# Kernel optimization log

Measured on AMD Instinct MI355X. Metric: run time of the kernel, lower is better.

Reference implementation:

```python
import jax, jax.numpy as jnp
import numpy as np

B, L, DIM, K, V = 512, 200, 256, 2048, 100000


def setup_inputs() -> dict:
    key = jax.random.key(0)
    k1, k2, k3, k4, k5 = jax.random.split(key, 5)
    return {
        "history_item_ids": jax.random.randint(k1, (B, L), 0, V, dtype=jnp.int32),
        "history_item_masks": jax.random.randint(k2, (B, L), 0, 3, dtype=jnp.int32),
        "embedding_table": jax.random.normal(k3, (V, DIM), dtype=jnp.float32) * 0.1,
        "code_book": jax.random.normal(k4, (K, DIM), dtype=jnp.float32) * 0.1,
        "W_enc": jax.random.normal(k5, (2 * DIM, DIM), dtype=jnp.float32) * 0.05,
        "b_enc": jnp.zeros((DIM,), dtype=jnp.float32),
    }


def reference(history_item_ids, history_item_masks, embedding_table, code_book, W_enc, b_enc):
    # mask: valid history positions (>= 1)
    mask = (history_item_masks >= 1).astype(jnp.float32)            # [B, L]
    emb = embedding_table[history_item_ids] * mask[:, :, None]      # [B, L, D]
    # masked mean over history (eps matches the tf 1e-9)
    hist_mean = emb.sum(axis=1) / (mask.sum(axis=1, keepdims=True) + 1e-9)  # [B, D]
    # VQ quantization: pairwise squared distances, argmin, codebook gather
    flat = emb.reshape(-1, emb.shape[-1])                           # [B*L, D]
    distances = (
        jnp.sum(flat * flat, axis=1, keepdims=True)
        + jnp.sum(code_book * code_book, axis=1)
        - 2.0 * flat @ code_book.T
    )                                                               # [B*L, K]
    idx = jnp.argmin(distances, axis=1)                             # [B*L]
    vq = code_book[idx].reshape(emb.shape)                          # [B, L, D] (== one_hot @ code_book)
    vq_mean = vq.sum(axis=1) / mask.sum(axis=-1)[:, None]           # [B, D] (no eps in tf vqvae)
    x = jnp.concatenate([vq_mean, hist_mean], axis=-1)              # [B, 2D]
    return x @ W_enc + b_enc                                        # encoder dense -> [B, D]
```

## Files before the change

### kernel.cpp

```cpp
#include <hip/hip_runtime.h>
#include <hip/hip_bf16.h>
#include <cstddef>
#include <cstdint>

#define B_  512
#define L_  200
#define D_  256
#define K_  2048
#define BL_ (B_ * L_)

typedef __bf16 bf16x8 __attribute__((ext_vector_type(8)));
typedef float  f32x16 __attribute__((ext_vector_type(16)));

#define GL_LDS(g, l) __builtin_amdgcn_global_load_lds(                          \
    (const __attribute__((address_space(1))) void*)(g),                         \
    (__attribute__((address_space(3))) void*)(l), 16, 0, 0)

__device__ inline ushort f2bf(float f) {
    union { float f; uint u; } a; a.f = f;
    uint r = a.u + 0x7FFFu + ((a.u >> 16) & 1u);
    return (ushort)(r >> 16);
}

__global__ __launch_bounds__(256) void prep_kernel(const float* __restrict__ cb,
                                                   float* __restrict__ cnorm,
                                                   float* __restrict__ cnormR,
                                                   ushort* __restrict__ cbbf) {
    int code = (blockIdx.x * 256 + threadIdx.x) >> 6;
    int lane = threadIdx.x & 63;
    float4 v = ((const float4*)(cb + (size_t)code * D_))[lane];
    float s = v.x * v.x + v.y * v.y + v.z * v.z + v.w * v.w;
    #pragma unroll
    for (int off = 32; off; off >>= 1) s += __shfl_down(s, off);
    union { ushort us[4]; uint2 u2; } pk;
    pk.us[0] = f2bf(v.x); pk.us[1] = f2bf(v.y); pk.us[2] = f2bf(v.z); pk.us[3] = f2bf(v.w);
    ((uint2*)(cbbf + (size_t)code * D_))[lane] = pk.u2;
    if (lane == 0) {
        cnorm[code] = s;
        int r = code & 31;
        int h = (r >> 2) & 1;
        int j = (r & 3) | ((r >> 3) << 2);
        cnormR[(code & ~31) | (h << 4) | j] = s + 16.0f;
    }
}

__global__ __launch_bounds__(256) void kstar_kernel(const float* __restrict__ cnorm,
                                                    int* __restrict__ kstar) {
    __shared__ unsigned long long red[4];
    const int t = threadIdx.x;
    unsigned long long best = ~0ull;
    #pragma unroll
    for (int i = 0; i < K_ / 256; ++i) {
        int k = i * 256 + t;
        unsigned long long key = (((unsigned long long)__float_as_uint(cnorm[k])) << 11) | (unsigned)k;
        best = best < key ? best : key;
    }
    #pragma unroll
    for (int off = 32; off; off >>= 1) {
        unsigned long long o = __shfl_down(best, off);
        best = best < o ? best : o;
    }
    if ((t & 63) == 0) red[t >> 6] = best;
    __syncthreads();
    if (t == 0) {
        unsigned long long b = red[0];
        for (int i = 1; i < 4; ++i) b = b < red[i] ? b : red[i];
        kstar[0] = (int)(b & 0x7FFull);
    }
}

struct CN4 { float4 a, b, c, d; };

__device__ inline CN4 ldcn(const float* p) {
    CN4 r;
    r.a = ((const float4*)p)[0];
    r.b = ((const float4*)p)[1];
    r.c = ((const float4*)p)[2];
    r.d = ((const float4*)p)[3];
    return r;
}

#define STAGE(CIDX, BUF) {                                                      \
    int wub = __builtin_amdgcn_readfirstlane((t >> 6) * 256);                   \
    _Pragma("unroll")                                                           \
    for (int i_ = 0; i_ < 4; ++i_) {                                            \
      int slot = wub + i_ * 64 + (t & 63);                                      \
      int n_ = slot >> 5, up_ = slot & 31;                                      \
      int u_ = up_ ^ (n_ & 7);                                                  \
      GL_LDS(cbbf + (((size_t)(((CIDX) << 5) + n_)) << 8) + (u_ << 3),          \
             (char*)(BUF) + (size_t)(wub + i_ * 64) * 16);                      \
    } }

#define PROCSEL(BUF, NC, CN) {                                                  \
    f32x16 A0, A1;                                                              \
    A0[0]=(CN).a.x; A0[1]=(CN).a.y; A0[2]=(CN).a.z; A0[3]=(CN).a.w;             \
    A0[4]=(CN).b.x; A0[5]=(CN).b.y; A0[6]=(CN).b.z; A0[7]=(CN).b.w;             \
    A0[8]=(CN).c.x; A0[9]=(CN).c.y; A0[10]=(CN).c.z; A0[11]=(CN).c.w;           \
    A0[12]=(CN).d.x; A0[13]=(CN).d.y; A0[14]=(CN).d.z; A0[15]=(CN).d.w;         \
    A1 = A0;                                                                    \
    _Pragma("unroll")                                                           \
    for (int s_ = 0; s_ < 16; ++s_) {                                           \
      bf16x8 aF = *(const bf16x8*)((const char*)(BUF) +                         \
                    (((l31 << 5) + ((2 * s_ + h) ^ swz)) << 4));                \
      A0 = __builtin_amdgcn_mfma_f32_32x32x16_bf16(aF, bfrag[0][s_], A0, 0,0,0);\
      A1 = __builtin_amdgcn_mfma_f32_32x32x16_bf16(aF, bfrag[1][s_], A1, 0,0,0);\
    }                                                                           \
    uint sb_ = (uint)((NC) << 5);                                               \
    _Pragma("unroll")                                                           \
    for (int jp_ = 0; jp_ < 8; ++jp_) {                                         \
      int j0_ = 2 * jp_, j1_ = 2 * jp_ + 1;                                     \
      uint c0_ = sb_ + (uint)((j0_ & 3) + 8 * (j0_ >> 2));                      \
      uint c1_ = sb_ + (uint)((j1_ & 3) + 8 * (j1_ >> 2));                      \
      {                                                                         \
        uint ka = (__float_as_uint(A0[j0_]) & 0xFFFFF800u) | (c0_ + h4);        \
        uint kb = (__float_as_uint(A0[j1_]) & 0xFFFFF800u) | (c1_ + h4);        \
        uint lo = min(ka, kb), hi = max(ka, kb);                                \
        uint tt = max(b1a, lo);                                                 \
        b1a = min(b1a, lo);                                                     \
        b2a = min(min(b2a, tt), hi);                                            \
      }                                                                         \
      {                                                                         \
        uint ka = (__float_as_uint(A1[j0_]) & 0xFFFFF800u) | (c0_ + h4);        \
        uint kb = (__float_as_uint(A1[j1_]) & 0xFFFFF800u) | (c1_ + h4);        \
        uint lo = min(ka, kb), hi = max(ka, kb);                                \
        uint tt = max(b1b, lo);                                                 \
        b1b = min(b1b, lo);                                                     \
        b2b = min(min(b2b, tt), hi);                                            \
      }                                                                         \
    } }

__global__ __launch_bounds__(256, 2) void gemm_top2_kernel(
    const int* __restrict__ ids, const int* __restrict__ masks,
    const float* __restrict__ table, const ushort* __restrict__ cbbf,
    const float* __restrict__ cnormR, uint2* __restrict__ cand) {

  __shared__ ushort cbuf0[32 * 256];
  __shared__ ushort cbuf1[32 * 256];

  const int t    = threadIdx.x;
  const int lane = t & 63;
  const int l31  = lane & 31;
  const int h    = lane >> 5;
  const int w    = t >> 6;
  const int ptile = blockIdx.x;
  const int swz  = l31 & 7;
  const uint h4  = (uint)(h << 2);

  bf16x8 bfrag[2][16];
  #pragma unroll
  for (int pt = 0; pt < 2; ++pt) {
    int pos = ptile * 256 + w * 64 + pt * 32 + l31;
    int id  = ids[pos];
    float m = (masks[pos] >= 1) ? -2.0f : 0.0f;
    const float* er = table + (size_t)id * D_ + 8 * h;
    #pragma unroll
    for (int s = 0; s < 16; ++s) {
      float4 x = *(const float4*)(er + 16 * s);
      float4 y = *(const float4*)(er + 16 * s + 4);
      bf16x8 b;
      b[0] = (__bf16)(x.x * m); b[1] = (__bf16)(x.y * m);
      b[2] = (__bf16)(x.z * m); b[3] = (__bf16)(x.w * m);
      b[4] = (__bf16)(y.x * m); b[5] = (__bf16)(y.y * m);
      b[6] = (__bf16)(y.z * m); b[7] = (__bf16)(y.w * m);
      bfrag[pt][s] = b;
    }
  }

  uint b1a = 0xFFFFFFFFu, b2a = 0xFFFFFFFFu;
  uint b1b = 0xFFFFFFFFu, b2b = 0xFFFFFFFFu;

  const float* cnh = cnormR;
  CN4 cnA = ldcn(cnh + 0 * 32 + h * 16);
  STAGE(0, cbuf0);
  __syncthreads();

  #pragma unroll 1
  for (int nc = 0; nc < 64; nc += 2) {
    CN4 cnB = ldcn(cnh + (nc + 1) * 32 + h * 16);
    STAGE(nc + 1, cbuf1);
    PROCSEL(cbuf0, nc, cnA);
    __syncthreads();
    if (nc + 2 < 64) {
      cnA = ldcn(cnh + (nc + 2) * 32 + h * 16);
      STAGE(nc + 2, cbuf0);
    }
    PROCSEL(cbuf1, nc + 1, cnB);
    __syncthreads();
  }

  {
    uint ob1 = __shfl_xor(b1a, 32), ob2 = __shfl_xor(b2a, 32);
    uint m1 = min(b1a, ob1);
    uint m2 = min(min(max(b1a, ob1), b2a), ob2);
    if (h == 0) cand[(size_t)(ptile * 256 + w * 64 + 0 * 32 + l31)] = make_uint2(m1, m2);
  }
  {
    uint ob1 = __shfl_xor(b1b, 32), ob2 = __shfl_xor(b2b, 32);
    uint m1 = min(b1b, ob1);
    uint m2 = min(min(max(b1b, ob1), b2b), ob2);
    if (h == 0) cand[(size_t)(ptile * 256 + w * 64 + 1 * 32 + l31)] = make_uint2(m1, m2);
  }
}

#define GRP 5

__global__ __launch_bounds__(256, 1) void tail_kernel(
    const int* __restrict__ ids, const int* __restrict__ masks,
    const float* __restrict__ table, const float* __restrict__ cb,
    const float* __restrict__ cnorm, const uint2* __restrict__ cand2,
    const int* __restrict__ kstar,
    float* __restrict__ gacc, int* __restrict__ gcnt) {

    __shared__ float red_vq[4][D_];
    __shared__ float red_e[4][D_];
    __shared__ int   redc[4];

    const int b    = blockIdx.x >> 1;
    const int half = blockIdx.x & 1;
    const int t = threadIdx.x;
    const int wv = t >> 6, lane = t & 63;

    const int ks = kstar[0];
    float4 ckstar = ((const float4*)(cb + (size_t)ks * D_))[lane];

    float4 vqa = make_float4(0.f, 0.f, 0.f, 0.f);
    float4 ea  = make_float4(0.f, 0.f, 0.f, 0.f);
    int cnta = 0, mcnt = 0;

    #pragma unroll 1
    for (int g = 0; g < 25 / GRP; ++g) {
        const int l0 = half * 100 + wv * 25 + g * GRP;

        uint2 kk[GRP];
        int   id[GRP];
        int   mk[GRP];
        #pragma unroll
        for (int j = 0; j < GRP; ++j) {
            int u = b * L_ + l0 + j;
            kk[j] = cand2[u];
            id[j] = ids[u];
            mk[j] = masks[u];
        }

        int k1[GRP], k2[GRP];
        bool valid[GRP], needy[GRP];
        #pragma unroll
        for (int j = 0; j < GRP; ++j) {
            uint g1 = kk[j].x;
            uint g2 = kk[j].y;
            k1[j] = (int)(g1 & 0x7FFu);
            k2[j] = (int)(g2 & 0x7FFu);
            valid[j] = (mk[j] >= 1);
            needy[j] = valid[j] && (((g2 & 0xFFFFF800u) - (g1 & 0xFFFFF800u)) < (3u << 11));
        }

        float4 e[GRP], c1[GRP], c2[GRP];
        #pragma unroll
        for (int j = 0; j < GRP; ++j)
            if (valid[j]) e[j] = ((const float4*)(table + (size_t)id[j] * D_))[lane];
        #pragma unroll
        for (int j = 0; j < GRP; ++j)
            if (valid[j]) c1[j] = ((const float4*)(cb + (size_t)k1[j] * D_))[lane];
        #pragma unroll
        for (int j = 0; j < GRP; ++j)
            if (needy[j]) c2[j] = ((const float4*)(cb + (size_t)k2[j] * D_))[lane];

        #pragma unroll
        for (int j = 0; j < GRP; ++j) {
            if (!valid[j]) { mcnt++; continue; }
            float4 ch = c1[j];
            if (needy[j]) {
                float d1 = fmaf(e[j].x, c1[j].x, fmaf(e[j].y, c1[j].y,
                            fmaf(e[j].z, c1[j].z, e[j].w * c1[j].w)));
                float d2 = fmaf(e[j].x, c2[j].x, fmaf(e[j].y, c2[j].y,
                            fmaf(e[j].z, c2[j].z, e[j].w * c2[j].w)));
                #pragma unroll
                for (int off = 32; off; off >>= 1) {
                    d1 += __shfl_xor(d1, off);
                    d2 += __shfl_xor(d2, off);
                }
                float s1 = cnorm[k1[j]] - 2.0f * d1;
                float s2 = cnorm[k2[j]] - 2.0f * d2;
                bool sel = (s2 < s1) || (s2 == s1 && k2[j] < k1[j]);
                ch = sel ? c2[j] : c1[j];
            }
            vqa.x += ch.x; vqa.y += ch.y; vqa.z += ch.z; vqa.w += ch.w;
            ea.x += e[j].x; ea.y += e[j].y; ea.z += e[j].z; ea.w += e[j].w;
            cnta++;
        }
    }

    float fm = (float)mcnt;
    vqa.x = fmaf(fm, ckstar.x, vqa.x);
    vqa.y = fmaf(fm, ckstar.y, vqa.y);
    vqa.z = fmaf(fm, ckstar.z, vqa.z);
    vqa.w = fmaf(fm, ckstar.w, vqa.w);

    *(float4*)&red_vq[wv][lane * 4] = vqa;
    *(float4*)&red_e[wv][lane * 4]  = ea;
    if (lane == 0) redc[wv] = cnta;
    __syncthreads();

    float vs = red_vq[0][t] + red_vq[1][t] + red_vq[2][t] + red_vq[3][t];
    float es = red_e[0][t] + red_e[1][t] + red_e[2][t] + red_e[3][t];
    atomicAdd(&gacc[(size_t)b * (2 * D_) + t], vs);
    atomicAdd(&gacc[(size_t)b * (2 * D_) + D_ + t], es);
    if (t == 0) atomicAdd(&gcnt[b], redc[0] + redc[1] + redc[2] + redc[3]);
}

__global__ __launch_bounds__(256) void dense_kernel(
    const float* __restrict__ gacc, const int* __restrict__ gcnt,
    const float* __restrict__ W, const float* __restrict__ bvec,
    float* __restrict__ out) {

    __shared__ float x[2 * D_];
    const int b = blockIdx.x;
    const int t = threadIdx.x;

    float fc = (float)gcnt[b];
    x[t]      = gacc[(size_t)b * (2 * D_) + t] / fc;
    x[D_ + t] = gacc[(size_t)b * (2 * D_) + D_ + t] / (fc + 1e-9f);
    __syncthreads();

    float acc = bvec[t];
    #pragma unroll 8
    for (int i = 0; i < 2 * D_; ++i)
        acc = fmaf(x[i], W[i * D_ + t], acc);
    out[(size_t)b * D_ + t] = acc;
}

extern "C" void kernel_launch(void* const* d_in, const int* in_sizes, int n_in,
                              void* d_out, int out_size, void* d_ws, size_t ws_size,
                              hipStream_t stream) {
    const int*   ids   = (const int*)  d_in[0];
    const int*   masks = (const int*)  d_in[1];
    const float* table = (const float*)d_in[2];
    const float* cb    = (const float*)d_in[3];
    const float* W     = (const float*)d_in[4];
    const float* bvec  = (const float*)d_in[5];
    float* out = (float*)d_out;

    char* p = (char*)d_ws;
    float*  cnorm  = (float*)p;             p += 8192;
    float*  cnormR = (float*)p;             p += 8192;
    ushort* cbbf   = (ushort*)p;            p += 1048576;
    uint2*  cand   = (uint2*)p;             p += (size_t)BL_ * 16;
    float*  gacc   = (float*)p;             p += (size_t)B_ * 2 * D_ * 4;
    int*    gcnt   = (int*)p;               p += B_ * 4;
    int*    kstar  = (int*)p;               p += 64;

    hipMemsetAsync(gacc, 0, (size_t)B_ * 2 * D_ * 4 + B_ * 4, stream);

    prep_kernel<<<K_ * 64 / 256, 256, 0, stream>>>(cb, cnorm, cnormR, cbbf);
    kstar_kernel<<<1, 256, 0, stream>>>(cnorm, kstar);
    gemm_top2_kernel<<<BL_ / 256, 256, 0, stream>>>(ids, masks, table, cbbf, cnormR, cand);
    tail_kernel<<<B_ * 2, 256, 0, stream>>>(ids, masks, table, cb, cnorm,
                                            cand, kstar, gacc, gcnt);
    dense_kernel<<<B_, 256, 0, stream>>>(gacc, gcnt, W, bvec, out);
}
```

Before: 317.7 us.

## Quad-buffer codebook staging with vmcnt waits and preload code norms into LDS

Replaces the double-buffered codebook chunk staging, which used two __syncthreads per pair of chunks, with a 4-buffer ring that prefetches three chunks ahead. Each iteration now does a single s_waitcnt vmcnt plus s_barrier. Per-chunk code-norm vectors are loaded once into LDS via global_load_lds instead of from global memory each chunk. This aims to hide load latency and remove barrier stalls, at the cost of more LDS (72KB vs 32KB), which may limit occupancy to fewer blocks per CU.

```diff
diff --git a/kernel.cpp b/kernel.cpp
--- a/kernel.cpp
+++ b/kernel.cpp
@@ -71,16 +71,7 @@
 
 struct CN4 { float4 a, b, c, d; };
 
-__device__ inline CN4 ldcn(const float* p) {
-    CN4 r;
-    r.a = ((const float4*)p)[0];
-    r.b = ((const float4*)p)[1];
-    r.c = ((const float4*)p)[2];
-    r.d = ((const float4*)p)[3];
-    return r;
-}
-
-#define STAGE(CIDX, BUF) {                                                      \
+#define STAGE(CIDX, BASE) {                                                     \
     int wub = __builtin_amdgcn_readfirstlane((t >> 6) * 256);                   \
     _Pragma("unroll")                                                           \
     for (int i_ = 0; i_ < 4; ++i_) {                                            \
@@ -88,10 +79,10 @@
       int n_ = slot >> 5, up_ = slot & 31;                                      \
       int u_ = up_ ^ (n_ & 7);                                                  \
       GL_LDS(cbbf + (((size_t)(((CIDX) << 5) + n_)) << 8) + (u_ << 3),          \
-             (char*)(BUF) + (size_t)(wub + i_ * 64) * 16);                      \
+             (char*)(BASE) + (size_t)(wub + i_ * 64) * 16);                     \
     } }
 
-#define PROCSEL(BUF, NC, CN) {                                                  \
+#define PROCSEL(BASE, NC, CN) {                                                 \
     f32x16 A0, A1;                                                              \
     A0[0]=(CN).a.x; A0[1]=(CN).a.y; A0[2]=(CN).a.z; A0[3]=(CN).a.w;             \
     A0[4]=(CN).b.x; A0[5]=(CN).b.y; A0[6]=(CN).b.z; A0[7]=(CN).b.w;             \
@@ -100,7 +91,7 @@
     A1 = A0;                                                                    \
     _Pragma("unroll")                                                           \
     for (int s_ = 0; s_ < 16; ++s_) {                                           \
-      bf16x8 aF = *(const bf16x8*)((const char*)(BUF) +                         \
+      bf16x8 aF = *(const bf16x8*)((const char*)(BASE) +                        \
                     (((l31 << 5) + ((2 * s_ + h) ^ swz)) << 4));                \
       A0 = __builtin_amdgcn_mfma_f32_32x32x16_bf16(aF, bfrag[0][s_], A0, 0,0,0);\
       A1 = __builtin_amdgcn_mfma_f32_32x32x16_bf16(aF, bfrag[1][s_], A1, 0,0,0);\
@@ -129,13 +120,17 @@
       }                                                                         \
     } }
 
+#define LDCN_LDS(NC, CN) {                                                      \
+    const float4* cp_ = (const float4*)(cnlds + ((NC) << 5) + (h << 4));        \
+    (CN).a = cp_[0]; (CN).b = cp_[1]; (CN).c = cp_[2]; (CN).d = cp_[3]; }
+
 __global__ __launch_bounds__(256, 2) void gemm_top2_kernel(
     const int* __restrict__ ids, const int* __restrict__ masks,
     const float* __restrict__ table, const ushort* __restrict__ cbbf,
     const float* __restrict__ cnormR, uint2* __restrict__ cand) {
 
-  __shared__ ushort cbuf0[32 * 256];
-  __shared__ ushort cbuf1[32 * 256];
+  __shared__ ushort cbuf[4 * 32 * 256];
+  __shared__ float  cnlds[2048];
 
   const int t    = threadIdx.x;
   const int lane = t & 63;
@@ -169,23 +164,47 @@
   uint b1a = 0xFFFFFFFFu, b2a = 0xFFFFFFFFu;
   uint b1b = 0xFFFFFFFFu, b2b = 0xFFFFFFFFu;
 
-  const float* cnh = cnormR;
-  CN4 cnA = ldcn(cnh + 0 * 32 + h * 16);
-  STAGE(0, cbuf0);
-  __syncthreads();
+  asm volatile("s_waitcnt vmcnt(0)" ::: "memory");
+  __builtin_amdgcn_sched_barrier(0);
+
+  {
+    int wub2 = __builtin_amdgcn_readfirstlane((t >> 6) * 128);
+    #pragma unroll
+    for (int i = 0; i < 2; ++i) {
+      int slot = wub2 + i * 64 + (t & 63);
+      GL_LDS(cnormR + (size_t)slot * 4, (char*)cnlds + (size_t)(wub2 + i * 64) * 16);
+    }
+  }
+  STAGE(0, (char*)cbuf);
+  STAGE(1, (char*)cbuf + 16384);
+  STAGE(2, (char*)cbuf + 32768);
 
   #pragma unroll 1
-  for (int nc = 0; nc < 64; nc += 2) {
-    CN4 cnB = ldcn(cnh + (nc + 1) * 32 + h * 16);
-    STAGE(nc + 1, cbuf1);
-    PROCSEL(cbuf0, nc, cnA);
-    __syncthreads();
-    if (nc + 2 < 64) {
-      cnA = ldcn(cnh + (nc + 2) * 32 + h * 16);
-      STAGE(nc + 2, cbuf0);
-    }
-    PROCSEL(cbuf1, nc + 1, cnB);
-    __syncthreads();
+  for (int nc = 0; nc < 62; ++nc) {
+    asm volatile("s_waitcnt vmcnt(8)" ::: "memory");
+    __builtin_amdgcn_s_barrier();
+    __builtin_amdgcn_sched_barrier(0);
+    if (nc <= 60) {
+      char* sb = (char*)cbuf + (size_t)(((nc + 3) & 3) * 16384);
+      STAGE(nc + 3, sb);
+    }
+    CN4 cn; LDCN_LDS(nc, cn);
+    char* rb = (char*)cbuf + (size_t)((nc & 3) * 16384);
+    PROCSEL(rb, nc, cn);
+  }
+  {
+    asm volatile("s_waitcnt vmcnt(4)" ::: "memory");
+    __builtin_amdgcn_s_barrier();
+    __builtin_amdgcn_sched_barrier(0);
+    CN4 cn; LDCN_LDS(62, cn);
+    PROCSEL((char*)cbuf + (size_t)((62 & 3) * 16384), 62, cn);
+  }
+  {
+    asm volatile("s_waitcnt vmcnt(0)" ::: "memory");
+    __builtin_amdgcn_s_barrier();
+    __builtin_amdgcn_sched_barrier(0);
+    CN4 cn; LDCN_LDS(63, cn);
+    PROCSEL((char*)cbuf + (size_t)((63 & 3) * 16384), 63, cn);
   }
 
   {
```

Result: no change. 314.4 us (-1.0%).

## Process two codebook chunks per pipeline stage and prefetch before embedding load

Applied to the files above, without the earlier changes.

Each double-buffer stage now holds two 32-code chunks (64 codes) instead of one, so the main loop runs half as many iterations and barriers, with four independent MFMA accumulator chains per step. The first codebook stage is issued before the embedding gather so that load overlaps fragment construction. This doubles LDS use per block (64 KB total) and adds accumulator registers, which may cut occupancy below the two blocks per CU the launch bounds request.

```diff
diff --git a/kernel.cpp b/kernel.cpp
--- a/kernel.cpp
+++ b/kernel.cpp
@@ -80,7 +80,7 @@
     return r;
 }
 
-#define STAGE(CIDX, BUF) {                                                      \
+#define STAGE(CIDX, BASE) {                                                     \
     int wub = __builtin_amdgcn_readfirstlane((t >> 6) * 256);                   \
     _Pragma("unroll")                                                           \
     for (int i_ = 0; i_ < 4; ++i_) {                                            \
@@ -88,23 +88,20 @@
       int n_ = slot >> 5, up_ = slot & 31;                                      \
       int u_ = up_ ^ (n_ & 7);                                                  \
       GL_LDS(cbbf + (((size_t)(((CIDX) << 5) + n_)) << 8) + (u_ << 3),          \
-             (char*)(BUF) + (size_t)(wub + i_ * 64) * 16);                      \
+             (char*)(BASE) + (size_t)(wub + i_ * 64) * 16);                     \
     } }
 
-#define PROCSEL(BUF, NC, CN) {                                                  \
-    f32x16 A0, A1;                                                              \
-    A0[0]=(CN).a.x; A0[1]=(CN).a.y; A0[2]=(CN).a.z; A0[3]=(CN).a.w;             \
-    A0[4]=(CN).b.x; A0[5]=(CN).b.y; A0[6]=(CN).b.z; A0[7]=(CN).b.w;             \
-    A0[8]=(CN).c.x; A0[9]=(CN).c.y; A0[10]=(CN).c.z; A0[11]=(CN).c.w;           \
-    A0[12]=(CN).d.x; A0[13]=(CN).d.y; A0[14]=(CN).d.z; A0[15]=(CN).d.w;         \
-    A1 = A0;                                                                    \
-    _Pragma("unroll")                                                           \
-    for (int s_ = 0; s_ < 16; ++s_) {                                           \
-      bf16x8 aF = *(const bf16x8*)((const char*)(BUF) +                         \
-                    (((l31 << 5) + ((2 * s_ + h) ^ swz)) << 4));                \
-      A0 = __builtin_amdgcn_mfma_f32_32x32x16_bf16(aF, bfrag[0][s_], A0, 0,0,0);\
-      A1 = __builtin_amdgcn_mfma_f32_32x32x16_bf16(aF, bfrag[1][s_], A1, 0,0,0);\
-    }                                                                           \
+#define STAGE2(DI, BASE) {                                                      \
+    STAGE(2 * (DI),     (char*)(BASE));                                         \
+    STAGE(2 * (DI) + 1, (char*)(BASE) + 16384); }
+
+#define ACCINIT(CN, A) {                                                        \
+    A[0]=(CN).a.x; A[1]=(CN).a.y; A[2]=(CN).a.z; A[3]=(CN).a.w;                 \
+    A[4]=(CN).b.x; A[5]=(CN).b.y; A[6]=(CN).b.z; A[7]=(CN).b.w;                 \
+    A[8]=(CN).c.x; A[9]=(CN).c.y; A[10]=(CN).c.z; A[11]=(CN).c.w;               \
+    A[12]=(CN).d.x; A[13]=(CN).d.y; A[14]=(CN).d.z; A[15]=(CN).d.w; }
+
+#define SELR(NC, A0, A1) {                                                      \
     uint sb_ = (uint)((NC) << 5);                                               \
     _Pragma("unroll")                                                           \
     for (int jp_ = 0; jp_ < 8; ++jp_) {                                         \
@@ -129,13 +126,32 @@
       }                                                                         \
     } }
 
+#define PROCSEL2(BASE, NC) {                                                    \
+    CN4 cnX = ldcn(cnormR + ((NC) << 5) + h * 16);                              \
+    CN4 cnY = ldcn(cnormR + (((NC) + 1) << 5) + h * 16);                        \
+    f32x16 A0, A1, C0, C1;                                                      \
+    ACCINIT(cnX, A0); A1 = A0;                                                  \
+    ACCINIT(cnY, C0); C1 = C0;                                                  \
+    _Pragma("unroll")                                                           \
+    for (int s_ = 0; s_ < 16; ++s_) {                                           \
+      int off_ = ((l31 << 5) + ((2 * s_ + h) ^ swz)) << 4;                      \
+      bf16x8 aF = *(const bf16x8*)((const char*)(BASE) + off_);                 \
+      bf16x8 aG = *(const bf16x8*)((const char*)(BASE) + 16384 + off_);         \
+      A0 = __builtin_amdgcn_mfma_f32_32x32x16_bf16(aF, bfrag[0][s_], A0, 0,0,0);\
+      A1 = __builtin_amdgcn_mfma_f32_32x32x16_bf16(aF, bfrag[1][s_], A1, 0,0,0);\
+      C0 = __builtin_amdgcn_mfma_f32_32x32x16_bf16(aG, bfrag[0][s_], C0, 0,0,0);\
+      C1 = __builtin_amdgcn_mfma_f32_32x32x16_bf16(aG, bfrag[1][s_], C1, 0,0,0);\
+    }                                                                           \
+    SELR((NC), A0, A1);                                                         \
+    SELR((NC) + 1, C0, C1); }
+
 __global__ __launch_bounds__(256, 2) void gemm_top2_kernel(
     const int* __restrict__ ids, const int* __restrict__ masks,
     const float* __restrict__ table, const ushort* __restrict__ cbbf,
     const float* __restrict__ cnormR, uint2* __restrict__ cand) {
 
-  __shared__ ushort cbuf0[32 * 256];
-  __shared__ ushort cbuf1[32 * 256];
+  __shared__ ushort cbuf0[2 * 32 * 256];
+  __shared__ ushort cbuf1[2 * 32 * 256];
 
   const int t    = threadIdx.x;
   const int lane = t & 63;
@@ -145,6 +161,8 @@
   const int ptile = blockIdx.x;
   const int swz  = l31 & 7;
   const uint h4  = (uint)(h << 2);
+
+  STAGE2(0, cbuf0);
 
   bf16x8 bfrag[2][16];
   #pragma unroll
@@ -169,22 +187,15 @@
   uint b1a = 0xFFFFFFFFu, b2a = 0xFFFFFFFFu;
   uint b1b = 0xFFFFFFFFu, b2b = 0xFFFFFFFFu;
 
-  const float* cnh = cnormR;
-  CN4 cnA = ldcn(cnh + 0 * 32 + h * 16);
-  STAGE(0, cbuf0);
   __syncthreads();
 
   #pragma unroll 1
-  for (int nc = 0; nc < 64; nc += 2) {
-    CN4 cnB = ldcn(cnh + (nc + 1) * 32 + h * 16);
-    STAGE(nc + 1, cbuf1);
-    PROCSEL(cbuf0, nc, cnA);
-    __syncthreads();
-    if (nc + 2 < 64) {
-      cnA = ldcn(cnh + (nc + 2) * 32 + h * 16);
-      STAGE(nc + 2, cbuf0);
-    }
-    PROCSEL(cbuf1, nc + 1, cnB);
+  for (int dt = 0; dt < 32; dt += 2) {
+    STAGE2(dt + 1, cbuf1);
+    PROCSEL2(cbuf0, dt * 2);
+    __syncthreads();
+    if (dt + 2 < 32) STAGE2(dt + 2, cbuf0);
+    PROCSEL2(cbuf1, dt * 2 + 2);
     __syncthreads();
   }
 
```

Result: slower. 358.2 us (+12.7%).
